# Kernel tuning notes

Hardware: AMD Instinct MI355X
Metric: run time of the kernel (lower is better)

## Reference

```python
import math
import jax, jax.numpy as jnp
import numpy as np

D_MODEL = 1024
N_HEADS = 16
HEAD_DIM = D_MODEL // N_HEADS
D_FF = 4096
N_LAYERS = 4
VOCAB = 2048
NUM_GROUPS = 15
CACHE_LEN = 17  # positions 0..16
EPS = 1e-6


def rmsnorm(x, w):
    return x * w * jax.lax.rsqrt(jnp.mean(x * x, axis=-1, keepdims=True) + EPS)


def rope(x, pos):
    # x: [S, H, hd], pos: [S] int
    hd = x.shape[-1]
    inv = 1.0 / (10000.0 ** (jnp.arange(0, hd, 2, dtype=jnp.float32) / hd))
    ang = pos[:, None].astype(jnp.float32) * inv  # [S, hd/2]
    cos = jnp.cos(ang)[:, None, :]
    sin = jnp.sin(ang)[:, None, :]
    x1, x2 = x[..., ::2], x[..., 1::2]
    return jnp.stack([x1 * cos - x2 * sin, x1 * sin + x2 * cos], axis=-1).reshape(x.shape)


def transformer_step(x, positions, kc, vc, wq, wk, wv, wo, w1, w2, w3, ln1, ln2, lnf):
    # x: [S, d]; positions: [S] contiguous; kc/vc: [L, H, T, hd] KV caches
    S = x.shape[0]
    cache_pos = jnp.arange(CACHE_LEN)
    mask = cache_pos[None, None, :] <= positions[None, :, None]  # causal vs cache [1,S,T]
    start = positions[0]
    for l in range(N_LAYERS):
        h = rmsnorm(x, ln1[l])
        q = rope((h @ wq[l].T).reshape(S, N_HEADS, HEAD_DIM), positions)
        k = rope((h @ wk[l].T).reshape(S, N_HEADS, HEAD_DIM), positions)
        v = (h @ wv[l].T).reshape(S, N_HEADS, HEAD_DIM)
        kc = jax.lax.dynamic_update_slice(kc, k.transpose(1, 0, 2)[None], (l, 0, start, 0))
        vc = jax.lax.dynamic_update_slice(vc, v.transpose(1, 0, 2)[None], (l, 0, start, 0))
        scores = jnp.einsum('shd,htd->hst', q, kc[l]) / math.sqrt(HEAD_DIM)
        p = jax.nn.softmax(jnp.where(mask, scores, -1e30), axis=-1)
        attn = jnp.einsum('hst,htd->shd', p, vc[l]).reshape(S, D_MODEL)
        x = x + attn @ wo[l].T
        h = rmsnorm(x, ln2[l])
        x = x + (jax.nn.silu(h @ w1[l].T) * (h @ w3[l].T)) @ w2[l].T
    return rmsnorm(x, lnf), kc, vc


def forward(talker_hidden, code_0_embed, wq, wk, wv, wo, w1, w2, w3, ln1, ln2, lnf, heads, embeds):
    kc = jnp.zeros((N_LAYERS, N_HEADS, CACHE_LEN, HEAD_DIM), jnp.float32)
    vc = kc
    # prefill: [talker_hidden; code_0_embed] at positions 0,1
    x0 = jnp.concatenate([talker_hidden[0], code_0_embed[0]], axis=0)  # [2, d]
    h, kc, vc = transformer_step(x0, jnp.arange(2), kc, vc, wq, wk, wv, wo, w1, w2, w3, ln1, ln2, lnf)
    hidden = h[-1:]  # last-token hidden [1, d]

    def step(carry, xs):
        hidden, kc, vc = carry
        head, etab, pos = xs  # head/etab: [V, d]
        logits = hidden @ head.T          # [1, V]
        code = jnp.argmax(logits, axis=-1)  # [1]
        emb = etab[code]                   # [1, d]
        nh, kc, vc = transformer_step(emb, pos[None], kc, vc, wq, wk, wv, wo, w1, w2, w3, ln1, ln2, lnf)
        return (nh, kc, vc), (logits[0], emb[0])

    (_, _, _), (all_logits, embs) = jax.lax.scan(
        step, (hidden, kc, vc), (heads, embeds, jnp.arange(2, 2 + NUM_GROUPS)))
    embed_sum = code_0_embed.reshape(-1) + embs.sum(0)
    return all_logits, embed_sum  # [15, V], [d]


def setup_inputs() -> dict:
    key = jax.random.key(0)
    ks = jax.random.split(key, 16)
    s = 0.02
    f32 = jnp.float32
    return {
        'talker_hidden': jax.random.normal(ks[0], (1, 1, D_MODEL), f32),
        'code_0_embed': jax.random.normal(ks[1], (1, 1, D_MODEL), f32),
        'wq': jax.random.normal(ks[2], (N_LAYERS, D_MODEL, D_MODEL), f32) * s,
        'wk': jax.random.normal(ks[3], (N_LAYERS, D_MODEL, D_MODEL), f32) * s,
        'wv': jax.random.normal(ks[4], (N_LAYERS, D_MODEL, D_MODEL), f32) * s,
        'wo': jax.random.normal(ks[5], (N_LAYERS, D_MODEL, D_MODEL), f32) * s,
        'w1': jax.random.normal(ks[6], (N_LAYERS, D_FF, D_MODEL), f32) * s,
        'w2': jax.random.normal(ks[7], (N_LAYERS, D_MODEL, D_FF), f32) * s,
        'w3': jax.random.normal(ks[8], (N_LAYERS, D_FF, D_MODEL), f32) * s,
        'ln1': jnp.ones((N_LAYERS, D_MODEL), f32),
        'ln2': jnp.ones((N_LAYERS, D_MODEL), f32),
        'lnf': jnp.ones((D_MODEL,), f32),
        'heads': jax.random.normal(ks[9], (NUM_GROUPS, VOCAB, D_MODEL), f32) * s,
        'embeds': jax.random.normal(ks[10], (NUM_GROUPS, VOCAB, D_MODEL), f32) * s,
    }


def reference(talker_hidden, code_0_embed, wq, wk, wv, wo, w1, w2, w3, ln1, ln2, lnf, heads, embeds):
    return forward(talker_hidden, code_0_embed, wq, wk, wv, wo, w1, w2, w3, ln1, ln2, lnf, heads, embeds)
```

## Files before the change

kernel.cpp:

```cpp
#include <hip/hip_runtime.h>
#include <math.h>

#define D_MODEL 1024
#define N_HEADS 16
#define HEAD_DIM 64
#define D_FF 4096
#define N_LAYERS 4
#define VOCAB 2048
#define NUM_GROUPS 15
#define CACHE_LEN 17
#define EPS 1e-6f
#define NB 256
#define NT 1024

typedef unsigned short ushort8v __attribute__((ext_vector_type(8)));

__device__ __forceinline__ float ldc(const float* p) {
  return __hip_atomic_load((float*)p, __ATOMIC_RELAXED, __HIP_MEMORY_SCOPE_AGENT);
}
__device__ __forceinline__ void stc(float* p, float v) {
  __hip_atomic_store(p, v, __ATOMIC_RELAXED, __HIP_MEMORY_SCOPE_AGENT);
}
__device__ __forceinline__ float2 ldc2(const float* p) {
  unsigned long long u = __hip_atomic_load((unsigned long long*)p, __ATOMIC_RELAXED,
                                           __HIP_MEMORY_SCOPE_AGENT);
  union { unsigned long long u; float2 f; } c;
  c.u = u;
  return c.f;
}
__device__ __forceinline__ void stc2(float* p, float a, float b) {
  union { unsigned long long u; float2 f; } c;
  c.f = make_float2(a, b);
  __hip_atomic_store((unsigned long long*)p, c.u, __ATOMIC_RELAXED,
                     __HIP_MEMORY_SCOPE_AGENT);
}
__device__ __forceinline__ void stc_u64(unsigned long long* p, unsigned long long v) {
  __hip_atomic_store(p, v, __ATOMIC_RELAXED, __HIP_MEMORY_SCOPE_AGENT);
}

__device__ __forceinline__ float bf2f(unsigned short u) {
  union { unsigned int i; float f; } c;
  c.i = ((unsigned int)u) << 16;
  return c.f;
}
__device__ __forceinline__ unsigned short f2bf(float f) {
  union { float f; unsigned int i; } c;
  c.f = f;
  unsigned int r = (c.i + 0x7fffu + ((c.i >> 16) & 1u)) >> 16;
  return (unsigned short)r;
}
__device__ __forceinline__ unsigned long long pack4bf(float4 v) {
  return (unsigned long long)f2bf(v.x) | ((unsigned long long)f2bf(v.y) << 16) |
         ((unsigned long long)f2bf(v.z) << 32) | ((unsigned long long)f2bf(v.w) << 48);
}

__device__ __forceinline__ float wred(float v) {
#pragma unroll
  for (int o = 32; o > 0; o >>= 1) v += __shfl_xor(v, o, 64);
  return v;
}

__device__ __forceinline__ void gsync(unsigned* bar, unsigned& gen) {
  __syncthreads();
  if (threadIdx.x == 0) {
    ++gen;
    unsigned* grp = bar + (blockIdx.x & 7) * 64;
    unsigned* master = bar + 512;
    unsigned* flag = bar + 576;
    bool released = false;
    unsigned old = __hip_atomic_fetch_add(grp, 1u, __ATOMIC_RELAXED,
                                          __HIP_MEMORY_SCOPE_AGENT);
    if (old == gen * (NB / 8) - 1) {
      unsigned om = __hip_atomic_fetch_add(master, 1u, __ATOMIC_RELAXED,
                                           __HIP_MEMORY_SCOPE_AGENT);
      if (om == gen * 8 - 1) {
        __hip_atomic_store(flag, gen, __ATOMIC_RELAXED, __HIP_MEMORY_SCOPE_AGENT);
        released = true;
      }
    }
    if (!released) {
      while (__hip_atomic_load(flag, __ATOMIC_RELAXED, __HIP_MEMORY_SCOPE_AGENT) < gen)
        __builtin_amdgcn_s_sleep(4);
    }
  }
  __syncthreads();
}

__device__ __forceinline__ void load_act_rms(const float* __restrict__ x,
                                             const float* __restrict__ ln, float* a) {
  int lane = threadIdx.x & 63;
  float ssq = 0.f;
#pragma unroll
  for (int it = 0; it < 2; ++it) {
    const float* xp = x + it * 512 + lane * 8;
#pragma unroll
    for (int c = 0; c < 8; c += 2) {
      float2 v = ldc2(xp + c);
      a[it * 8 + c] = v.x;
      a[it * 8 + c + 1] = v.y;
      ssq = fmaf(v.x, v.x, fmaf(v.y, v.y, ssq));
    }
  }
  float scale = rsqrtf(wred(ssq) * (1.f / D_MODEL) + EPS);
  const float4* lv = (const float4*)ln;
#pragma unroll
  for (int it = 0; it < 2; ++it) {
    float4 l0 = lv[it * 128 + lane * 2];
    float4 l1 = lv[it * 128 + lane * 2 + 1];
    a[it * 8 + 0] *= l0.x * scale;
    a[it * 8 + 1] *= l0.y * scale;
    a[it * 8 + 2] *= l0.z * scale;
    a[it * 8 + 3] *= l0.w * scale;
    a[it * 8 + 4] *= l1.x * scale;
    a[it * 8 + 5] *= l1.y * scale;
    a[it * 8 + 6] *= l1.z * scale;
    a[it * 8 + 7] *= l1.w * scale;
  }
}

template <typename WT, int NIT>
__device__ __forceinline__ float dot_cached(const WT* __restrict__ wrow, const float* a) {
  int lane = threadIdx.x & 63;
  float acc = 0.f;
  if constexpr (sizeof(WT) == 2) {
    const ushort8v* w8 = (const ushort8v*)wrow;
#pragma unroll
    for (int it = 0; it < NIT; ++it) {
      ushort8v w = w8[it * 64 + lane];
#pragma unroll
      for (int c = 0; c < 8; ++c) acc = fmaf(bf2f(w[c]), a[it * 8 + c], acc);
    }
  } else {
    const float4* w4 = (const float4*)wrow;
#pragma unroll
    for (int it = 0; it < NIT; ++it) {
      float4 b0 = w4[it * 128 + lane * 2];
      float4 b1 = w4[it * 128 + lane * 2 + 1];
      acc = fmaf(b0.x, a[it * 8 + 0], acc);
      acc = fmaf(b0.y, a[it * 8 + 1], acc);
      acc = fmaf(b0.z, a[it * 8 + 2], acc);
      acc = fmaf(b0.w, a[it * 8 + 3], acc);
      acc = fmaf(b1.x, a[it * 8 + 4], acc);
      acc = fmaf(b1.y, a[it * 8 + 5], acc);
      acc = fmaf(b1.z, a[it * 8 + 6], acc);
      acc = fmaf(b1.w, a[it * 8 + 7], acc);
    }
  }
  return wred(acc);
}

template <typename WT, int NIT>
__device__ __forceinline__ float dot_lds(const WT* __restrict__ wrow,
                                         const float* __restrict__ act) {
  int lane = threadIdx.x & 63;
  const float4* av = (const float4*)act;
  float acc = 0.f;
  if constexpr (sizeof(WT) == 2) {
    const ushort8v* w8 = (const ushort8v*)wrow;
#pragma unroll
    for (int it = 0; it < NIT; ++it) {
      ushort8v w = w8[it * 64 + lane];
      float4 v0 = av[it * 128 + lane * 2];
      float4 v1 = av[it * 128 + lane * 2 + 1];
      acc = fmaf(bf2f(w[0]), v0.x, acc);
      acc = fmaf(bf2f(w[1]), v0.y, acc);
      acc = fmaf(bf2f(w[2]), v0.z, acc);
      acc = fmaf(bf2f(w[3]), v0.w, acc);
      acc = fmaf(bf2f(w[4]), v1.x, acc);
      acc = fmaf(bf2f(w[5]), v1.y, acc);
      acc = fmaf(bf2f(w[6]), v1.z, acc);
      acc = fmaf(bf2f(w[7]), v1.w, acc);
    }
  } else {
    const float4* w4 = (const float4*)wrow;
#pragma unroll
    for (int it = 0; it < NIT; ++it) {
      float4 b0 = w4[it * 128 + lane * 2];
      float4 b1 = w4[it * 128 + lane * 2 + 1];
      float4 v0 = av[it * 128 + lane * 2];
      float4 v1 = av[it * 128 + lane * 2 + 1];
      acc = fmaf(b0.x, v0.x, acc);
      acc = fmaf(b0.y, v0.y, acc);
      acc = fmaf(b0.z, v0.z, acc);
      acc = fmaf(b0.w, v0.w, acc);
      acc = fmaf(b1.x, v1.x, acc);
      acc = fmaf(b1.y, v1.y, acc);
      acc = fmaf(b1.z, v1.z, acc);
      acc = fmaf(b1.w, v1.w, acc);
    }
  }
  return wred(acc);
}

template <typename WT>
__device__ __forceinline__ float dot_ffq(const WT* __restrict__ wrow,
                                         const float* __restrict__ ffq) {
  int lane = threadIdx.x & 63;
  float acc = 0.f;
#pragma unroll
  for (int it = 0; it < 2; ++it) {
    const float* fp = ffq + it * 512 + lane * 8;
    float2 v0 = ldc2(fp), v1 = ldc2(fp + 2), v2 = ldc2(fp + 4), v3 = ldc2(fp + 6);
    if constexpr (sizeof(WT) == 2) {
      ushort8v w = ((const ushort8v*)wrow)[it * 64 + lane];
      acc = fmaf(bf2f(w[0]), v0.x, acc);
      acc = fmaf(bf2f(w[1]), v0.y, acc);
      acc = fmaf(bf2f(w[2]), v1.x, acc);
      acc = fmaf(bf2f(w[3]), v1.y, acc);
      acc = fmaf(bf2f(w[4]), v2.x, acc);
      acc = fmaf(bf2f(w[5]), v2.y, acc);
      acc = fmaf(bf2f(w[6]), v3.x, acc);
      acc = fmaf(bf2f(w[7]), v3.y, acc);
    } else {
      const float4* w4 = (const float4*)wrow;
      float4 b0 = w4[it * 128 + lane * 2];
      float4 b1 = w4[it * 128 + lane * 2 + 1];
      acc = fmaf(b0.x, v0.x, acc);
      acc = fmaf(b0.y, v0.y, acc);
      acc = fmaf(b0.z, v1.x, acc);
      acc = fmaf(b0.w, v1.y, acc);
      acc = fmaf(b1.x, v2.x, acc);
      acc = fmaf(b1.y, v2.y, acc);
      acc = fmaf(b1.z, v3.x, acc);
      acc = fmaf(b1.w, v3.y, acc);
    }
  }
  return wred(acc);
}

struct Sh {
  float attn[2][D_MODEL];
  float red[32];
  float bval[16];
  int bidx[16];
  int code;
};

__device__ __forceinline__ int block_argmax(const float* __restrict__ lbuf, Sh& sh) {
  int tid = threadIdx.x, lane = tid & 63, wv_ = tid >> 6;
  float v0 = ldc(lbuf + tid);
  int i0 = tid;
  float v1 = ldc(lbuf + tid + 1024);
  if (v1 > v0) { v0 = v1; i0 = tid + 1024; }
#pragma unroll
  for (int o = 32; o > 0; o >>= 1) {
    float v2 = __shfl_xor(v0, o, 64);
    int i2 = __shfl_xor(i0, o, 64);
    if (v2 > v0 || (v2 == v0 && i2 < i0)) { v0 = v2; i0 = i2; }
  }
  if (lane == 0) { sh.bval[wv_] = v0; sh.bidx[wv_] = i0; }
  __syncthreads();
  if (tid == 0) {
    float b = sh.bval[0];
    int bi = sh.bidx[0];
#pragma unroll
    for (int w = 1; w < 16; ++w) {
      float v = sh.bval[w];
      int i = sh.bidx[w];
      if (v > b || (v == b && i < bi)) { b = v; bi = i; }
    }
    sh.code = bi;
  }
  __syncthreads();
  return sh.code;
}

__device__ __forceinline__ void conv_arr(const float* __restrict__ src,
                                         unsigned long long* __restrict__ dst,
                                         size_t n8) {
  const float4* s4 = (const float4*)src;
  for (size_t i = (size_t)blockIdx.x * NT + threadIdx.x; i < n8; i += (size_t)NB * NT) {
    float4 a = s4[2 * i];
    float4 b = s4[2 * i + 1];
    stc_u64(dst + 2 * i, pack4bf(a));
    stc_u64(dst + 2 * i + 1, pack4bf(b));
  }
}

struct KParams {
  const float *th, *c0, *ln1, *ln2, *lnf, *heads, *embeds;
  const float *fwq, *fwk, *fwv, *fwo, *fw1, *fw2, *fw3;
  unsigned short *bwq, *bwk, *bwv, *bwo, *bw1, *bw2, *bw3;
  float *out, *x, *qb, *ff, *lbuf, *esum, *kc, *vc;
  unsigned* bar;
};

template <int BF> struct WSel;
template <> struct WSel<1> { using T = unsigned short; };
template <> struct WSel<0> { using T = float; };

__global__ void k_zero(unsigned* bar) {
  if (threadIdx.x < 640) bar[threadIdx.x] = 0;
}

template <int BF>
__global__ __launch_bounds__(NT, 4) void mega(KParams P) {
  using WT = typename WSel<BF>::T;
  __shared__ Sh sh;
  unsigned gen = 0;
  const int tid = threadIdx.x, lane = tid & 63, wv_ = tid >> 6;

  const WT* wq = BF ? (const WT*)P.bwq : (const WT*)P.fwq;
  const WT* wk = BF ? (const WT*)P.bwk : (const WT*)P.fwk;
  const WT* wv = BF ? (const WT*)P.bwv : (const WT*)P.fwv;
  const WT* wo = BF ? (const WT*)P.bwo : (const WT*)P.fwo;
  const WT* w1 = BF ? (const WT*)P.bw1 : (const WT*)P.fw1;
  const WT* w2 = BF ? (const WT*)P.bw2 : (const WT*)P.fw2;
  const WT* w3 = BF ? (const WT*)P.bw3 : (const WT*)P.fw3;

  const size_t QKVO = (size_t)N_LAYERS * D_MODEL * D_MODEL;
  const size_t FFW = (size_t)N_LAYERS * D_FF * D_MODEL;

  if constexpr (BF) {
    conv_arr(P.fwq, (unsigned long long*)P.bwq, QKVO / 8);
    conv_arr(P.fwk, (unsigned long long*)P.bwk, QKVO / 8);
    conv_arr(P.fwv, (unsigned long long*)P.bwv, QKVO / 8);
    conv_arr(P.fwo, (unsigned long long*)P.bwo, QKVO / 8);
    conv_arr(P.fw1, (unsigned long long*)P.bw1, FFW / 8);
    conv_arr(P.fw3, (unsigned long long*)P.bw3, FFW / 8);
    conv_arr(P.fw2, (unsigned long long*)P.bw2, FFW / 8);
  }
  if (blockIdx.x == 0) {
    stc(&P.x[tid], P.th[tid]);
    stc(&P.x[D_MODEL + tid], P.c0[tid]);
    P.esum[tid] = P.c0[tid];
  }
  gsync(P.bar, gen);

  auto qkv_phase = [&](const float* hin, int S, int start, const float* ln,
                       const WT* Wq, const WT* Wk, const WT* Wv, float* kcl,
                       float* vcl) {
    int R = blockIdx.x * 12 + wv_;
    int m = R >> 10, rr = R & 1023;
    int h = rr >> 6, dd = rr & 63;
    const WT* wrow = ((m == 0) ? Wq : (m == 1) ? Wk : Wv) + (size_t)rr * D_MODEL;
    for (int s = 0; s < S; ++s) {
      if (wv_ < 12) {
        float a[16];
        load_act_rms(hin + s * D_MODEL, ln, a);
        float d = dot_cached<WT, 2>(wrow, a);
        if (m == 2) {
          if (lane == 0) stc(&vcl[(h * CACHE_LEN + start + s) * HEAD_DIM + dd], d);
        } else {
          if (lane == 0) sh.red[s * 16 + wv_] = d;
        }
      }
    }
    __syncthreads();
    if (wv_ < 12 && m < 2 && !(rr & 1) && lane == 0) {
      int i = dd >> 1;
      float inv = powf(10000.f, -(float)(2 * i) / 64.f);
      for (int s = 0; s < S; ++s) {
        int pos = start + s;
        float d0 = sh.red[s * 16 + wv_];
        float d1 = sh.red[s * 16 + wv_ + 1];
        float ang = (float)pos * inv;
        float c = cosf(ang), sn = sinf(ang);
        float o0 = d0 * c - d1 * sn;
        float o1 = d0 * sn + d1 * c;
        if (m == 0) stc2(&P.qb[s * D_MODEL + rr], o0, o1);
        else stc2(&kcl[(h * CACHE_LEN + pos) * HEAD_DIM + dd], o0, o1);
      }
    }
  };

  auto aw_phase = [&](int S, int start, const WT* Wo, const float* kcl,
                      const float* vcl) {
    int h = wv_;
    for (int s = 0; s < S; ++s) {
      int pos = start + s;
      float qd = ldc(&P.qb[s * D_MODEL + h * HEAD_DIM + lane]);
      float sc = -1e30f;
      for (int t = 0; t <= pos; ++t) {
        float sum = wred(qd * ldc(&kcl[(h * CACHE_LEN + t) * HEAD_DIM + lane]));
        if (lane == t) sc = sum * 0.125f;
      }
      float mx = sc;
#pragma unroll
      for (int o = 32; o > 0; o >>= 1) mx = fmaxf(mx, __shfl_xor(mx, o, 64));
      float e = (lane <= pos) ? expf(sc - mx) : 0.f;
      float den = wred(e);
      float pr = e / den;
      float acc = 0.f;
      for (int t = 0; t <= pos; ++t)
        acc = fmaf(__shfl(pr, t, 64),
                   ldc(&vcl[(h * CACHE_LEN + t) * HEAD_DIM + lane]), acc);
      sh.attn[s][h * HEAD_DIM + lane] = acc;
    }
    __syncthreads();
    if (wv_ < 8) {
      int rr = wv_ >> 1, q = wv_ & 1;
      int row = blockIdx.x * 4 + rr;
      const WT* wrow = Wo + (size_t)row * D_MODEL;
      for (int s = 0; s < S; ++s) {
        float part = dot_lds<WT, 1>(wrow + q * 512, &sh.attn[s][q * 512]);
        if (lane == 0) sh.red[s * 16 + wv_] = part;
      }
    }
    __syncthreads();
    if (tid < 4 * S) {
      int s = tid >> 2, rr = tid & 3;
      float* xp = &P.x[s * D_MODEL + blockIdx.x * 4 + rr];
      stc(xp, ldc(xp) + sh.red[s * 16 + rr * 2] + sh.red[s * 16 + rr * 2 + 1]);
    }
  };

  auto ffup_phase = [&](int S, const float* ln, const WT* W1, const WT* W3) {
    int j = blockIdx.x * 16 + wv_;
    const WT* r1 = W1 + (size_t)j * D_MODEL;
    const WT* r3 = W3 + (size_t)j * D_MODEL;
    for (int s = 0; s < S; ++s) {
      float a[16];
      load_act_rms(P.x + s * D_MODEL, ln, a);
      float g = dot_cached<WT, 2>(r1, a);
      float u = dot_cached<WT, 2>(r3, a);
      if (lane == 0) stc(&P.ff[s * D_FF + j], (g / (1.f + expf(-g))) * u);
    }
  };

  auto ffdown_phase = [&](int S, const WT* W2) {
    int rr = wv_ >> 2, q = wv_ & 3;
    int row = blockIdx.x * 4 + rr;
    const WT* wrow = W2 + (size_t)row * D_FF;
    for (int s = 0; s < S; ++s) {
      float pt = dot_ffq<WT>(wrow + q * 1024, P.ff + s * D_FF + q * 1024);
      if (lane == 0) sh.red[s * 16 + wv_] = pt;
    }
    __syncthreads();
    if (tid < 4 * S) {
      int s = tid >> 2, rr2 = tid & 3;
      float v = sh.red[s * 16 + rr2 * 4] + sh.red[s * 16 + rr2 * 4 + 1] +
                sh.red[s * 16 + rr2 * 4 + 2] + sh.red[s * 16 + rr2 * 4 + 3];
      float* xp = &P.x[s * D_MODEL + blockIdx.x * 4 + rr2];
      stc(xp, ldc(xp) + v);
    }
  };

  auto logits_phase = [&](int row, const float* head, float* outg) {
    if (wv_ < 8) {
      int j = blockIdx.x * 8 + wv_;
      float a[16];
      load_act_rms(P.x + row * D_MODEL, P.lnf, a);
      float d = dot_cached<float, 2>(head + (size_t)j * D_MODEL, a);
      if (lane == 0) {
        stc(&P.lbuf[j], d);
        outg[j] = d;
      }
    }
  };

  auto full_step = [&](int S, int start, bool am, const float* etab) {
    for (int l = 0; l < N_LAYERS; ++l) {
      const WT* Wq = wq + (size_t)l * D_MODEL * D_MODEL;
      const WT* Wk = wk + (size_t)l * D_MODEL * D_MODEL;
      const WT* Wv = wv + (size_t)l * D_MODEL * D_MODEL;
      const WT* Wo = wo + (size_t)l * D_MODEL * D_MODEL;
      const WT* W1 = w1 + (size_t)l * D_FF * D_MODEL;
      const WT* W2 = w2 + (size_t)l * D_FF * D_MODEL;
      const WT* W3 = w3 + (size_t)l * D_FF * D_MODEL;
      float* kcl = P.kc + (size_t)l * N_HEADS * CACHE_LEN * HEAD_DIM;
      float* vcl = P.vc + (size_t)l * N_HEADS * CACHE_LEN * HEAD_DIM;
      const float* hin = P.x;
      if (am && l == 0) {
        int code = block_argmax(P.lbuf, sh);
        hin = etab + (size_t)code * D_MODEL;
        if (blockIdx.x == 0) {
          float e = hin[tid];
          stc(&P.x[tid], e);
          P.esum[tid] += e;
        }
      }
      qkv_phase(hin, S, start, P.ln1 + l * D_MODEL, Wq, Wk, Wv, kcl, vcl);
      gsync(P.bar, gen);
      aw_phase(S, start, Wo, kcl, vcl);
      gsync(P.bar, gen);
      ffup_phase(S, P.ln2 + l * D_MODEL, W1, W3);
      gsync(P.bar, gen);
      ffdown_phase(S, W2);
      gsync(P.bar, gen);
    }
  };

  full_step(2, 0, false, nullptr);

  for (int g = 0; g < NUM_GROUPS; ++g) {
    logits_phase(g == 0 ? 1 : 0, P.heads + (size_t)g * VOCAB * D_MODEL,
                 P.out + (size_t)g * VOCAB);
    gsync(P.bar, gen);
    if (g < NUM_GROUPS - 1) {
      full_step(1, 2 + g, true, P.embeds + (size_t)g * VOCAB * D_MODEL);
    } else {
      if (blockIdx.x == 0) {
        int code = block_argmax(P.lbuf, sh);
        const float* emb =
            P.embeds + (size_t)g * VOCAB * D_MODEL + (size_t)code * D_MODEL;
        P.out[(size_t)NUM_GROUPS * VOCAB + tid] = P.esum[tid] + emb[tid];
      }
    }
  }
}

extern "C" void kernel_launch(void* const* d_in, const int* in_sizes, int n_in,
                              void* d_out, int out_size, void* d_ws, size_t ws_size,
                              hipStream_t stream) {
  KParams P;
  P.th = (const float*)d_in[0];
  P.c0 = (const float*)d_in[1];
  P.fwq = (const float*)d_in[2];
  P.fwk = (const float*)d_in[3];
  P.fwv = (const float*)d_in[4];
  P.fwo = (const float*)d_in[5];
  P.fw1 = (const float*)d_in[6];
  P.fw2 = (const float*)d_in[7];
  P.fw3 = (const float*)d_in[8];
  P.ln1 = (const float*)d_in[9];
  P.ln2 = (const float*)d_in[10];
  P.lnf = (const float*)d_in[11];
  P.heads = (const float*)d_in[12];
  P.embeds = (const float*)d_in[13];
  P.out = (float*)d_out;

  const size_t QKVO = (size_t)N_LAYERS * D_MODEL * D_MODEL;
  const size_t FFW = (size_t)N_LAYERS * D_FF * D_MODEL;
  const size_t W_ELEMS = 4 * QKVO + 3 * FFW;
  const size_t SCRATCH = 2048 + 2048 + 8192 + 2048 + 1024 + 69632 + 69632;
  const size_t NEED = W_ELEMS * 2 + (SCRATCH + 640) * 4;

  float* fs;
  int use_bf16 = (ws_size >= NEED);
  if (use_bf16) {
    unsigned short* wb = (unsigned short*)d_ws;
    P.bwq = wb;
    P.bwk = wb + QKVO;
    P.bwv = wb + 2 * QKVO;
    P.bwo = wb + 3 * QKVO;
    P.bw1 = wb + 4 * QKVO;
    P.bw3 = wb + 4 * QKVO + FFW;
    P.bw2 = wb + 4 * QKVO + 2 * FFW;
    fs = (float*)(wb + W_ELEMS);
  } else {
    P.bwq = P.bwk = P.bwv = P.bwo = P.bw1 = P.bw2 = P.bw3 = nullptr;
    fs = (float*)d_ws;
  }
  P.x = fs;
  P.qb = fs + 2048;
  P.ff = fs + 4096;
  P.lbuf = fs + 12288;
  P.esum = fs + 14336;
  P.kc = fs + 15360;
  P.vc = fs + 84992;
  P.bar = (unsigned*)(fs + SCRATCH);

  k_zero<<<1, 1024, 0, stream>>>(P.bar);
  void* args[] = {&P};
  if (use_bf16) {
    hipLaunchCooperativeKernel(reinterpret_cast<void*>(&mega<1>), dim3(NB), dim3(NT),
                               args, 0, stream);
  } else {
    hipLaunchCooperativeKernel(reinterpret_cast<void*>(&mega<0>), dim3(NB), dim3(NT),
                               args, 0, stream);
  }
}
```

Before: 1.984 ms.

## Split grid barrier and prefetch next-phase weights into registers during sync

Replaces the hierarchical atomic-counter grid barrier with a split flag barrier: each block publishes its generation in its own padded slot, and 64 lanes poll all 256 slots. Between arrival and wait, each wave issues register loads of the weight rows it needs in the next phase (Wo, W1/W3, W2, the next layer's QKV, or the next logits head), so weight fetch latency overlaps barrier wait. Attention scoring is unrolled over the full cache length with masking, and logits now use all 16 waves with half-rows instead of 8 waves. The cost is more register pressure from the prefetched rows, extra polling traffic, and a larger flag area that needs zeroing.

```diff
diff --git a/kernel.cpp b/kernel.cpp
--- a/kernel.cpp
+++ b/kernel.cpp
@@ -37,6 +37,9 @@
 __device__ __forceinline__ void stc_u64(unsigned long long* p, unsigned long long v) {
   __hip_atomic_store(p, v, __ATOMIC_RELAXED, __HIP_MEMORY_SCOPE_AGENT);
 }
+__device__ __forceinline__ unsigned ldu(const unsigned* p) {
+  return __hip_atomic_load((unsigned*)p, __ATOMIC_RELAXED, __HIP_MEMORY_SCOPE_AGENT);
+}
 
 __device__ __forceinline__ float bf2f(unsigned short u) {
   union { unsigned int i; float f; } c;
@@ -59,31 +62,140 @@
   for (int o = 32; o > 0; o >>= 1) v += __shfl_xor(v, o, 64);
   return v;
 }
-
-__device__ __forceinline__ void gsync(unsigned* bar, unsigned& gen) {
+__device__ __forceinline__ float wredmax(float v) {
+#pragma unroll
+  for (int o = 32; o > 0; o >>= 1) v = fmaxf(v, __shfl_xor(v, o, 64));
+  return v;
+}
+
+__device__ __forceinline__ void gsync_begin(unsigned* flags, unsigned gen) {
   __syncthreads();
-  if (threadIdx.x == 0) {
-    ++gen;
-    unsigned* grp = bar + (blockIdx.x & 7) * 64;
-    unsigned* master = bar + 512;
-    unsigned* flag = bar + 576;
-    bool released = false;
-    unsigned old = __hip_atomic_fetch_add(grp, 1u, __ATOMIC_RELAXED,
-                                          __HIP_MEMORY_SCOPE_AGENT);
-    if (old == gen * (NB / 8) - 1) {
-      unsigned om = __hip_atomic_fetch_add(master, 1u, __ATOMIC_RELAXED,
-                                           __HIP_MEMORY_SCOPE_AGENT);
-      if (om == gen * 8 - 1) {
-        __hip_atomic_store(flag, gen, __ATOMIC_RELAXED, __HIP_MEMORY_SCOPE_AGENT);
-        released = true;
-      }
-    }
-    if (!released) {
-      while (__hip_atomic_load(flag, __ATOMIC_RELAXED, __HIP_MEMORY_SCOPE_AGENT) < gen)
-        __builtin_amdgcn_s_sleep(4);
+  if (threadIdx.x == 0)
+    __hip_atomic_store(flags + (size_t)blockIdx.x * 16u, gen, __ATOMIC_RELAXED,
+                       __HIP_MEMORY_SCOPE_AGENT);
+}
+__device__ __forceinline__ void gsync_end(unsigned* flags, unsigned gen) {
+  if (threadIdx.x < 64) {
+    const unsigned* f = flags + (size_t)threadIdx.x * 16u;
+    for (;;) {
+      unsigned a0 = ldu(f);
+      unsigned a1 = ldu(f + 64 * 16);
+      unsigned a2 = ldu(f + 128 * 16);
+      unsigned a3 = ldu(f + 192 * 16);
+      if (a0 >= gen && a1 >= gen && a2 >= gen && a3 >= gen) break;
+      __builtin_amdgcn_s_sleep(2);
     }
   }
   __syncthreads();
+}
+
+template <typename WT> struct Row;
+template <> struct Row<unsigned short> { ushort8v x0, x1; };
+template <> struct Row<float> { float4 x0, x1, x2, x3; };
+template <typename WT> struct HalfR;
+template <> struct HalfR<unsigned short> { ushort8v v; };
+template <> struct HalfR<float> { float4 a, b; };
+
+template <typename WT>
+__device__ __forceinline__ Row<WT> ldrow(const WT* __restrict__ w) {
+  int lane = threadIdx.x & 63;
+  Row<WT> r;
+  if constexpr (sizeof(WT) == 2) {
+    const ushort8v* w8 = (const ushort8v*)w;
+    r.x0 = w8[lane];
+    r.x1 = w8[64 + lane];
+  } else {
+    const float4* w4 = (const float4*)w;
+    r.x0 = w4[lane * 2];
+    r.x1 = w4[lane * 2 + 1];
+    r.x2 = w4[128 + lane * 2];
+    r.x3 = w4[128 + lane * 2 + 1];
+  }
+  return r;
+}
+template <typename WT>
+__device__ __forceinline__ HalfR<WT> ldhalf(const WT* __restrict__ w) {
+  int lane = threadIdx.x & 63;
+  HalfR<WT> r;
+  if constexpr (sizeof(WT) == 2) {
+    r.v = ((const ushort8v*)w)[lane];
+  } else {
+    const float4* w4 = (const float4*)w;
+    r.a = w4[lane * 2];
+    r.b = w4[lane * 2 + 1];
+  }
+  return r;
+}
+
+template <typename WT>
+__device__ __forceinline__ float dotrow(const Row<WT>& r, const float* a) {
+  float acc = 0.f;
+  if constexpr (sizeof(WT) == 2) {
+#pragma unroll
+    for (int c = 0; c < 8; ++c) acc = fmaf(bf2f(r.x0[c]), a[c], acc);
+#pragma unroll
+    for (int c = 0; c < 8; ++c) acc = fmaf(bf2f(r.x1[c]), a[8 + c], acc);
+  } else {
+    acc = fmaf(r.x0.x, a[0], acc);
+    acc = fmaf(r.x0.y, a[1], acc);
+    acc = fmaf(r.x0.z, a[2], acc);
+    acc = fmaf(r.x0.w, a[3], acc);
+    acc = fmaf(r.x1.x, a[4], acc);
+    acc = fmaf(r.x1.y, a[5], acc);
+    acc = fmaf(r.x1.z, a[6], acc);
+    acc = fmaf(r.x1.w, a[7], acc);
+    acc = fmaf(r.x2.x, a[8], acc);
+    acc = fmaf(r.x2.y, a[9], acc);
+    acc = fmaf(r.x2.z, a[10], acc);
+    acc = fmaf(r.x2.w, a[11], acc);
+    acc = fmaf(r.x3.x, a[12], acc);
+    acc = fmaf(r.x3.y, a[13], acc);
+    acc = fmaf(r.x3.z, a[14], acc);
+    acc = fmaf(r.x3.w, a[15], acc);
+  }
+  return wred(acc);
+}
+
+template <typename WT>
+__device__ __forceinline__ float dothalf_mem(const HalfR<WT>& r,
+                                             const float* __restrict__ act) {
+  int lane = threadIdx.x & 63;
+  const float4* av = (const float4*)act;
+  float4 v0 = av[lane * 2], v1 = av[lane * 2 + 1];
+  float acc = 0.f;
+  if constexpr (sizeof(WT) == 2) {
+    acc = fmaf(bf2f(r.v[0]), v0.x, acc);
+    acc = fmaf(bf2f(r.v[1]), v0.y, acc);
+    acc = fmaf(bf2f(r.v[2]), v0.z, acc);
+    acc = fmaf(bf2f(r.v[3]), v0.w, acc);
+    acc = fmaf(bf2f(r.v[4]), v1.x, acc);
+    acc = fmaf(bf2f(r.v[5]), v1.y, acc);
+    acc = fmaf(bf2f(r.v[6]), v1.z, acc);
+    acc = fmaf(bf2f(r.v[7]), v1.w, acc);
+  } else {
+    acc = fmaf(r.a.x, v0.x, acc);
+    acc = fmaf(r.a.y, v0.y, acc);
+    acc = fmaf(r.a.z, v0.z, acc);
+    acc = fmaf(r.a.w, v0.w, acc);
+    acc = fmaf(r.b.x, v1.x, acc);
+    acc = fmaf(r.b.y, v1.y, acc);
+    acc = fmaf(r.b.z, v1.z, acc);
+    acc = fmaf(r.b.w, v1.w, acc);
+  }
+  return wred(acc);
+}
+
+__device__ __forceinline__ float dothalf_reg(const HalfR<float>& r, const float* a8) {
+  float acc = 0.f;
+  acc = fmaf(r.a.x, a8[0], acc);
+  acc = fmaf(r.a.y, a8[1], acc);
+  acc = fmaf(r.a.z, a8[2], acc);
+  acc = fmaf(r.a.w, a8[3], acc);
+  acc = fmaf(r.b.x, a8[4], acc);
+  acc = fmaf(r.b.y, a8[5], acc);
+  acc = fmaf(r.b.z, a8[6], acc);
+  acc = fmaf(r.b.w, a8[7], acc);
+  return wred(acc);
 }
 
 __device__ __forceinline__ void load_act_rms(const float* __restrict__ x,
@@ -118,114 +230,18 @@
   }
 }
 
-template <typename WT, int NIT>
-__device__ __forceinline__ float dot_cached(const WT* __restrict__ wrow, const float* a) {
+__device__ __forceinline__ void load_ffseg(const float* __restrict__ base, float* a) {
   int lane = threadIdx.x & 63;
-  float acc = 0.f;
-  if constexpr (sizeof(WT) == 2) {
-    const ushort8v* w8 = (const ushort8v*)wrow;
-#pragma unroll
-    for (int it = 0; it < NIT; ++it) {
-      ushort8v w = w8[it * 64 + lane];
-#pragma unroll
-      for (int c = 0; c < 8; ++c) acc = fmaf(bf2f(w[c]), a[it * 8 + c], acc);
-    }
-  } else {
-    const float4* w4 = (const float4*)wrow;
-#pragma unroll
-    for (int it = 0; it < NIT; ++it) {
-      float4 b0 = w4[it * 128 + lane * 2];
-      float4 b1 = w4[it * 128 + lane * 2 + 1];
-      acc = fmaf(b0.x, a[it * 8 + 0], acc);
-      acc = fmaf(b0.y, a[it * 8 + 1], acc);
-      acc = fmaf(b0.z, a[it * 8 + 2], acc);
-      acc = fmaf(b0.w, a[it * 8 + 3], acc);
-      acc = fmaf(b1.x, a[it * 8 + 4], acc);
-      acc = fmaf(b1.y, a[it * 8 + 5], acc);
-      acc = fmaf(b1.z, a[it * 8 + 6], acc);
-      acc = fmaf(b1.w, a[it * 8 + 7], acc);
-    }
-  }
-  return wred(acc);
-}
-
-template <typename WT, int NIT>
-__device__ __forceinline__ float dot_lds(const WT* __restrict__ wrow,
-                                         const float* __restrict__ act) {
-  int lane = threadIdx.x & 63;
-  const float4* av = (const float4*)act;
-  float acc = 0.f;
-  if constexpr (sizeof(WT) == 2) {
-    const ushort8v* w8 = (const ushort8v*)wrow;
-#pragma unroll
-    for (int it = 0; it < NIT; ++it) {
-      ushort8v w = w8[it * 64 + lane];
-      float4 v0 = av[it * 128 + lane * 2];
-      float4 v1 = av[it * 128 + lane * 2 + 1];
-      acc = fmaf(bf2f(w[0]), v0.x, acc);
-      acc = fmaf(bf2f(w[1]), v0.y, acc);
-      acc = fmaf(bf2f(w[2]), v0.z, acc);
-      acc = fmaf(bf2f(w[3]), v0.w, acc);
-      acc = fmaf(bf2f(w[4]), v1.x, acc);
-      acc = fmaf(bf2f(w[5]), v1.y, acc);
-      acc = fmaf(bf2f(w[6]), v1.z, acc);
-      acc = fmaf(bf2f(w[7]), v1.w, acc);
-    }
-  } else {
-    const float4* w4 = (const float4*)wrow;
-#pragma unroll
-    for (int it = 0; it < NIT; ++it) {
-      float4 b0 = w4[it * 128 + lane * 2];
-      float4 b1 = w4[it * 128 + lane * 2 + 1];
-      float4 v0 = av[it * 128 + lane * 2];
-      float4 v1 = av[it * 128 + lane * 2 + 1];
-      acc = fmaf(b0.x, v0.x, acc);
-      acc = fmaf(b0.y, v0.y, acc);
-      acc = fmaf(b0.z, v0.z, acc);
-      acc = fmaf(b0.w, v0.w, acc);
-      acc = fmaf(b1.x, v1.x, acc);
-      acc = fmaf(b1.y, v1.y, acc);
-      acc = fmaf(b1.z, v1.z, acc);
-      acc = fmaf(b1.w, v1.w, acc);
-    }
-  }
-  return wred(acc);
-}
-
-template <typename WT>
-__device__ __forceinline__ float dot_ffq(const WT* __restrict__ wrow,
-                                         const float* __restrict__ ffq) {
-  int lane = threadIdx.x & 63;
-  float acc = 0.f;
 #pragma unroll
   for (int it = 0; it < 2; ++it) {
-    const float* fp = ffq + it * 512 + lane * 8;
-    float2 v0 = ldc2(fp), v1 = ldc2(fp + 2), v2 = ldc2(fp + 4), v3 = ldc2(fp + 6);
-    if constexpr (sizeof(WT) == 2) {
-      ushort8v w = ((const ushort8v*)wrow)[it * 64 + lane];
-      acc = fmaf(bf2f(w[0]), v0.x, acc);
-      acc = fmaf(bf2f(w[1]), v0.y, acc);
-      acc = fmaf(bf2f(w[2]), v1.x, acc);
-      acc = fmaf(bf2f(w[3]), v1.y, acc);
-      acc = fmaf(bf2f(w[4]), v2.x, acc);
-      acc = fmaf(bf2f(w[5]), v2.y, acc);
-      acc = fmaf(bf2f(w[6]), v3.x, acc);
-      acc = fmaf(bf2f(w[7]), v3.y, acc);
-    } else {
-      const float4* w4 = (const float4*)wrow;
-      float4 b0 = w4[it * 128 + lane * 2];
-      float4 b1 = w4[it * 128 + lane * 2 + 1];
-      acc = fmaf(b0.x, v0.x, acc);
-      acc = fmaf(b0.y, v0.y, acc);
-      acc = fmaf(b0.z, v1.x, acc);
-      acc = fmaf(b0.w, v1.y, acc);
-      acc = fmaf(b1.x, v2.x, acc);
-      acc = fmaf(b1.y, v2.y, acc);
-      acc = fmaf(b1.z, v3.x, acc);
-      acc = fmaf(b1.w, v3.y, acc);
-    }
-  }
-  return wred(acc);
+    const float* p = base + it * 512 + lane * 8;
+#pragma unroll
+    for (int c = 0; c < 8; c += 2) {
+      float2 v = ldc2(p + c);
+      a[it * 8 + c] = v.x;
+      a[it * 8 + c + 1] = v.y;
+    }
+  }
 }
 
 struct Sh {
@@ -290,7 +306,8 @@
 template <> struct WSel<0> { using T = float; };
 
 __global__ void k_zero(unsigned* bar) {
-  if (threadIdx.x < 640) bar[threadIdx.x] = 0;
+  int i = blockIdx.x * 1024 + threadIdx.x;
+  if (i < 4096) bar[i] = 0;
 }
 
 template <int BF>
@@ -299,6 +316,7 @@
   __shared__ Sh sh;
   unsigned gen = 0;
   const int tid = threadIdx.x, lane = tid & 63, wv_ = tid >> 6;
+  const int bid = blockIdx.x;
 
   const WT* wq = BF ? (const WT*)P.bwq : (const WT*)P.fwq;
   const WT* wk = BF ? (const WT*)P.bwk : (const WT*)P.fwk;
@@ -307,6 +325,23 @@
   const WT* w1 = BF ? (const WT*)P.bw1 : (const WT*)P.fw1;
   const WT* w2 = BF ? (const WT*)P.bw2 : (const WT*)P.fw2;
   const WT* w3 = BF ? (const WT*)P.bw3 : (const WT*)P.fw3;
+
+  const int R_q = bid * 12 + wv_;
+  const int m_q = R_q >> 10;
+  const int rr_q = R_q & 1023;
+  const int h_q = rr_q >> 6, dd_q = rr_q & 63;
+  const int wo_r = (wv_ >> 1) & 3, wo_h = wv_ & 1;
+  const int ff_j = bid * 16 + wv_;
+  const int w2_r = wv_ >> 2, w2_q = wv_ & 3;
+  const int lg_r = wv_ >> 1, lg_h = wv_ & 1;
+
+  auto qkvrow = [&](int l) -> const WT* {
+    const WT* W = (m_q == 0) ? wq : (m_q == 1) ? wk : wv;
+    return W + (size_t)l * D_MODEL * D_MODEL + (size_t)rr_q * D_MODEL;
+  };
+
+  Row<WT> pQ{};
+  HalfR<float> pH{};
 
   const size_t QKVO = (size_t)N_LAYERS * D_MODEL * D_MODEL;
   const size_t FFW = (size_t)N_LAYERS * D_FF * D_MODEL;
@@ -320,35 +355,33 @@
     conv_arr(P.fw3, (unsigned long long*)P.bw3, FFW / 8);
     conv_arr(P.fw2, (unsigned long long*)P.bw2, FFW / 8);
   }
-  if (blockIdx.x == 0) {
+  if (bid == 0) {
     stc(&P.x[tid], P.th[tid]);
     stc(&P.x[D_MODEL + tid], P.c0[tid]);
     P.esum[tid] = P.c0[tid];
   }
-  gsync(P.bar, gen);
+  ++gen;
+  gsync_begin(P.bar, gen);
+  gsync_end(P.bar, gen);
+  pQ = ldrow(qkvrow(0));
 
   auto qkv_phase = [&](const float* hin, int S, int start, const float* ln,
-                       const WT* Wq, const WT* Wk, const WT* Wv, float* kcl,
-                       float* vcl) {
-    int R = blockIdx.x * 12 + wv_;
-    int m = R >> 10, rr = R & 1023;
-    int h = rr >> 6, dd = rr & 63;
-    const WT* wrow = ((m == 0) ? Wq : (m == 1) ? Wk : Wv) + (size_t)rr * D_MODEL;
+                       float* kcl, float* vcl) {
     for (int s = 0; s < S; ++s) {
       if (wv_ < 12) {
         float a[16];
         load_act_rms(hin + s * D_MODEL, ln, a);
-        float d = dot_cached<WT, 2>(wrow, a);
-        if (m == 2) {
-          if (lane == 0) stc(&vcl[(h * CACHE_LEN + start + s) * HEAD_DIM + dd], d);
-        } else {
-          if (lane == 0) sh.red[s * 16 + wv_] = d;
+        float d = dotrow(pQ, a);
+        if (m_q >= 2) {
+          if (lane == 0) stc(&vcl[(h_q * CACHE_LEN + start + s) * HEAD_DIM + dd_q], d);
+        } else if (lane == 0) {
+          sh.red[s * 16 + wv_] = d;
         }
       }
     }
     __syncthreads();
-    if (wv_ < 12 && m < 2 && !(rr & 1) && lane == 0) {
-      int i = dd >> 1;
+    if (wv_ < 12 && m_q < 2 && !(rr_q & 1) && lane == 0) {
+      int i = dd_q >> 1;
       float inv = powf(10000.f, -(float)(2 * i) / 64.f);
       for (int s = 0; s < S; ++s) {
         int pos = start + s;
@@ -358,72 +391,70 @@
         float c = cosf(ang), sn = sinf(ang);
         float o0 = d0 * c - d1 * sn;
         float o1 = d0 * sn + d1 * c;
-        if (m == 0) stc2(&P.qb[s * D_MODEL + rr], o0, o1);
-        else stc2(&kcl[(h * CACHE_LEN + pos) * HEAD_DIM + dd], o0, o1);
+        if (m_q == 0) stc2(&P.qb[s * D_MODEL + rr_q], o0, o1);
+        else stc2(&kcl[(h_q * CACHE_LEN + pos) * HEAD_DIM + dd_q], o0, o1);
       }
     }
   };
 
-  auto aw_phase = [&](int S, int start, const WT* Wo, const float* kcl,
-                      const float* vcl) {
-    int h = wv_;
+  auto aw_phase = [&](int S, int start, const float* kcl, const float* vcl,
+                      const HalfR<WT>& pWo) {
     for (int s = 0; s < S; ++s) {
       int pos = start + s;
-      float qd = ldc(&P.qb[s * D_MODEL + h * HEAD_DIM + lane]);
+      float qd = ldc(&P.qb[s * D_MODEL + wv_ * HEAD_DIM + lane]);
+      float prd[CACHE_LEN];
+#pragma unroll
+      for (int t = 0; t < CACHE_LEN; ++t)
+        prd[t] = qd * ldc(&kcl[(wv_ * CACHE_LEN + t) * HEAD_DIM + lane]);
       float sc = -1e30f;
-      for (int t = 0; t <= pos; ++t) {
-        float sum = wred(qd * ldc(&kcl[(h * CACHE_LEN + t) * HEAD_DIM + lane]));
-        if (lane == t) sc = sum * 0.125f;
-      }
-      float mx = sc;
-#pragma unroll
-      for (int o = 32; o > 0; o >>= 1) mx = fmaxf(mx, __shfl_xor(mx, o, 64));
+#pragma unroll
+      for (int t = 0; t < CACHE_LEN; ++t) {
+        float s_ = wred(prd[t]);
+        if (lane == t) sc = s_ * 0.125f;
+      }
+      float mx = wredmax(lane <= pos ? sc : -1e30f);
       float e = (lane <= pos) ? expf(sc - mx) : 0.f;
       float den = wred(e);
       float pr = e / den;
       float acc = 0.f;
-      for (int t = 0; t <= pos; ++t)
-        acc = fmaf(__shfl(pr, t, 64),
-                   ldc(&vcl[(h * CACHE_LEN + t) * HEAD_DIM + lane]), acc);
-      sh.attn[s][h * HEAD_DIM + lane] = acc;
+#pragma unroll
+      for (int t = 0; t < CACHE_LEN; ++t) {
+        float v = ldc(&vcl[(wv_ * CACHE_LEN + t) * HEAD_DIM + lane]);
+        bool ok = t <= pos;
+        acc = fmaf(ok ? __shfl(pr, t, 64) : 0.f, ok ? v : 0.f, acc);
+      }
+      sh.attn[s][wv_ * HEAD_DIM + lane] = acc;
     }
     __syncthreads();
     if (wv_ < 8) {
-      int rr = wv_ >> 1, q = wv_ & 1;
-      int row = blockIdx.x * 4 + rr;
-      const WT* wrow = Wo + (size_t)row * D_MODEL;
       for (int s = 0; s < S; ++s) {
-        float part = dot_lds<WT, 1>(wrow + q * 512, &sh.attn[s][q * 512]);
+        float part = dothalf_mem(pWo, &sh.attn[s][wo_h * 512]);
         if (lane == 0) sh.red[s * 16 + wv_] = part;
       }
     }
     __syncthreads();
     if (tid < 4 * S) {
       int s = tid >> 2, rr = tid & 3;
-      float* xp = &P.x[s * D_MODEL + blockIdx.x * 4 + rr];
+      float* xp = &P.x[s * D_MODEL + bid * 4 + rr];
       stc(xp, ldc(xp) + sh.red[s * 16 + rr * 2] + sh.red[s * 16 + rr * 2 + 1]);
     }
   };
 
-  auto ffup_phase = [&](int S, const float* ln, const WT* W1, const WT* W3) {
-    int j = blockIdx.x * 16 + wv_;
-    const WT* r1 = W1 + (size_t)j * D_MODEL;
-    const WT* r3 = W3 + (size_t)j * D_MODEL;
+  auto ffup_phase = [&](int S, const float* ln, const Row<WT>& p1, const Row<WT>& p3) {
     for (int s = 0; s < S; ++s) {
       float a[16];
       load_act_rms(P.x + s * D_MODEL, ln, a);
-      float g = dot_cached<WT, 2>(r1, a);
-      float u = dot_cached<WT, 2>(r3, a);
-      if (lane == 0) stc(&P.ff[s * D_FF + j], (g / (1.f + expf(-g))) * u);
+      float g = dotrow(p1, a);
+      float u = dotrow(p3, a);
+      if (lane == 0) stc(&P.ff[s * D_FF + ff_j], (g / (1.f + expf(-g))) * u);
     }
   };
 
-  auto ffdown_phase = [&](int S, const WT* W2) {
-    int rr = wv_ >> 2, q = wv_ & 3;
-    int row = blockIdx.x * 4 + rr;
-    const WT* wrow = W2 + (size_t)row * D_FF;
+  auto ffdown_phase = [&](int S, const Row<WT>& pW2) {
     for (int s = 0; s < S; ++s) {
-      float pt = dot_ffq<WT>(wrow + q * 1024, P.ff + s * D_FF + q * 1024);
+      float a[16];
+      load_ffseg(P.ff + s * D_FF + w2_q * 1024, a);
+      float pt = dotrow(pW2, a);
       if (lane == 0) sh.red[s * 16 + wv_] = pt;
     }
     __syncthreads();
@@ -431,66 +462,91 @@
       int s = tid >> 2, rr2 = tid & 3;
       float v = sh.red[s * 16 + rr2 * 4] + sh.red[s * 16 + rr2 * 4 + 1] +
                 sh.red[s * 16 + rr2 * 4 + 2] + sh.red[s * 16 + rr2 * 4 + 3];
-      float* xp = &P.x[s * D_MODEL + blockIdx.x * 4 + rr2];
+      float* xp = &P.x[s * D_MODEL + bid * 4 + rr2];
       stc(xp, ldc(xp) + v);
     }
   };
 
-  auto logits_phase = [&](int row, const float* head, float* outg) {
-    if (wv_ < 8) {
-      int j = blockIdx.x * 8 + wv_;
-      float a[16];
-      load_act_rms(P.x + row * D_MODEL, P.lnf, a);
-      float d = dot_cached<float, 2>(head + (size_t)j * D_MODEL, a);
-      if (lane == 0) {
-        stc(&P.lbuf[j], d);
-        outg[j] = d;
-      }
+  auto logits_phase = [&](int row, float* outg) {
+    float a[16];
+    load_act_rms(P.x + row * D_MODEL, P.lnf, a);
+    float d = dothalf_reg(pH, a + lg_h * 8);
+    if (lane == 0) sh.red[wv_] = d;
+    __syncthreads();
+    if (tid < 8) {
+      int j2 = bid * 8 + tid;
+      float v = sh.red[tid * 2] + sh.red[tid * 2 + 1];
+      stc(&P.lbuf[j2], v);
+      outg[j2] = v;
     }
   };
 
-  auto full_step = [&](int S, int start, bool am, const float* etab) {
+  auto full_step = [&](int S, int start, bool am, const float* etab,
+                       const float* next_head) {
     for (int l = 0; l < N_LAYERS; ++l) {
-      const WT* Wq = wq + (size_t)l * D_MODEL * D_MODEL;
-      const WT* Wk = wk + (size_t)l * D_MODEL * D_MODEL;
-      const WT* Wv = wv + (size_t)l * D_MODEL * D_MODEL;
-      const WT* Wo = wo + (size_t)l * D_MODEL * D_MODEL;
-      const WT* W1 = w1 + (size_t)l * D_FF * D_MODEL;
-      const WT* W2 = w2 + (size_t)l * D_FF * D_MODEL;
-      const WT* W3 = w3 + (size_t)l * D_FF * D_MODEL;
+      const WT* Wo_l = wo + (size_t)l * D_MODEL * D_MODEL;
+      const WT* W1_l = w1 + (size_t)l * D_FF * D_MODEL;
+      const WT* W2_l = w2 + (size_t)l * D_MODEL * D_FF;
+      const WT* W3_l = w3 + (size_t)l * D_FF * D_MODEL;
       float* kcl = P.kc + (size_t)l * N_HEADS * CACHE_LEN * HEAD_DIM;
       float* vcl = P.vc + (size_t)l * N_HEADS * CACHE_LEN * HEAD_DIM;
       const float* hin = P.x;
       if (am && l == 0) {
         int code = block_argmax(P.lbuf, sh);
+        hin = P.embeds == etab ? etab : etab;
         hin = etab + (size_t)code * D_MODEL;
-        if (blockIdx.x == 0) {
+        if (bid == 0) {
           float e = hin[tid];
           stc(&P.x[tid], e);
           P.esum[tid] += e;
         }
       }
-      qkv_phase(hin, S, start, P.ln1 + l * D_MODEL, Wq, Wk, Wv, kcl, vcl);
-      gsync(P.bar, gen);
-      aw_phase(S, start, Wo, kcl, vcl);
-      gsync(P.bar, gen);
-      ffup_phase(S, P.ln2 + l * D_MODEL, W1, W3);
-      gsync(P.bar, gen);
-      ffdown_phase(S, W2);
-      gsync(P.bar, gen);
+      qkv_phase(hin, S, start, P.ln1 + l * D_MODEL, kcl, vcl);
+      ++gen;
+      gsync_begin(P.bar, gen);
+      HalfR<WT> pWo = ldhalf(Wo_l + (size_t)(bid * 4 + wo_r) * D_MODEL + wo_h * 512);
+      __builtin_amdgcn_sched_barrier(0);
+      gsync_end(P.bar, gen);
+      aw_phase(S, start, kcl, vcl, pWo);
+      ++gen;
+      gsync_begin(P.bar, gen);
+      Row<WT> p1 = ldrow(W1_l + (size_t)ff_j * D_MODEL);
+      Row<WT> p3 = ldrow(W3_l + (size_t)ff_j * D_MODEL);
+      __builtin_amdgcn_sched_barrier(0);
+      gsync_end(P.bar, gen);
+      ffup_phase(S, P.ln2 + l * D_MODEL, p1, p3);
+      ++gen;
+      gsync_begin(P.bar, gen);
+      Row<WT> pW2 = ldrow(W2_l + (size_t)(bid * 4 + w2_r) * D_FF + w2_q * 1024);
+      __builtin_amdgcn_sched_barrier(0);
+      gsync_end(P.bar, gen);
+      ffdown_phase(S, pW2);
+      ++gen;
+      gsync_begin(P.bar, gen);
+      if (l < N_LAYERS - 1) {
+        pQ = ldrow(qkvrow(l + 1));
+      } else {
+        pH = ldhalf<float>(next_head + (size_t)(bid * 8 + lg_r) * D_MODEL + lg_h * 512);
+      }
+      __builtin_amdgcn_sched_barrier(0);
+      gsync_end(P.bar, gen);
     }
   };
 
-  full_step(2, 0, false, nullptr);
+  full_step(2, 0, false, nullptr, P.heads);
 
   for (int g = 0; g < NUM_GROUPS; ++g) {
-    logits_phase(g == 0 ? 1 : 0, P.heads + (size_t)g * VOCAB * D_MODEL,
-                 P.out + (size_t)g * VOCAB);
-    gsync(P.bar, gen);
+    logits_phase(g == 0 ? 1 : 0, P.out + (size_t)g * VOCAB);
+    ++gen;
+    gsync_begin(P.bar, gen);
+    pQ = ldrow(qkvrow(0));
+    __builtin_amdgcn_sched_barrier(0);
+    gsync_end(P.bar, gen);
     if (g < NUM_GROUPS - 1) {
-      full_step(1, 2 + g, true, P.embeds + (size_t)g * VOCAB * D_MODEL);
+      full_step(1, 2 + g, true, P.embeds + (size_t)g * VOCAB * D_MODEL,
+                P.heads + (size_t)(g + 1) * VOCAB * D_MODEL);
     } else {
-      if (blockIdx.x == 0) {
+      if (bid == 0) {
         int code = block_argmax(P.lbuf, sh);
         const float* emb =
             P.embeds + (size_t)g * VOCAB * D_MODEL + (size_t)code * D_MODEL;
@@ -524,7 +580,7 @@
   const size_t FFW = (size_t)N_LAYERS * D_FF * D_MODEL;
   const size_t W_ELEMS = 4 * QKVO + 3 * FFW;
   const size_t SCRATCH = 2048 + 2048 + 8192 + 2048 + 1024 + 69632 + 69632;
-  const size_t NEED = W_ELEMS * 2 + (SCRATCH + 640) * 4;
+  const size_t NEED = W_ELEMS * 2 + SCRATCH * 4 + 4096 * 4;
 
   float* fs;
   int use_bf16 = (ws_size >= NEED);
@@ -551,7 +607,7 @@
   P.vc = fs + 84992;
   P.bar = (unsigned*)(fs + SCRATCH);
 
-  k_zero<<<1, 1024, 0, stream>>>(P.bar);
+  k_zero<<<4, 1024, 0, stream>>>(P.bar);
   void* args[] = {&P};
   if (use_bf16) {
     hipLaunchCooperativeKernel(reinterpret_cast<void*>(&mega<1>), dim3(NB), dim3(NT),
```

Measured after the change: 2.071 ms. 4.4% more time.
